# Optimization experiments

Measured on AMD Instinct MI355X. Metric: run time of the kernel, lower is better.

The kernel has to match this reference:

```python
import jax, jax.numpy as jnp
import numpy as np

N_NODES = 2000
GCN_OUT = 8
HID = 256
N_STEPS_OUT = 4


def setup_inputs() -> dict:
    key = jax.random.key(0)
    ks = jax.random.split(key, 16)
    B, S, N, E, F, H = 32, 24, N_NODES, 16000, GCN_OUT, HID
    I = F * N  # LSTM input size = gcn_out_features * num_nodes
    s = 0.05
    inp = {
        "x_sequences": jax.random.normal(ks[0], (B, S, N), jnp.float32),
        "edge_index": jax.random.randint(ks[1], (B, S, 2, E), 0, N, jnp.int32),
        "edge_distances": jax.random.uniform(ks[2], (B, S, E), jnp.float32),
        # CustomGCNLayer params (linear 1->F)
        "W_gcn": jax.random.normal(ks[3], (1, F), jnp.float32) * s,
        "b_gcn": jnp.zeros((F,), jnp.float32),
        # 2-layer LSTM (PyTorch layout: [4H, in], gate order i,f,g,o)
        "Wih0": jax.random.normal(ks[4], (4 * H, I), jnp.float32) * s,
        "Whh0": jax.random.normal(ks[5], (4 * H, H), jnp.float32) * s,
        "bih0": jnp.zeros((4 * H,), jnp.float32),
        "bhh0": jnp.zeros((4 * H,), jnp.float32),
        "Wih1": jax.random.normal(ks[6], (4 * H, H), jnp.float32) * s,
        "Whh1": jax.random.normal(ks[7], (4 * H, H), jnp.float32) * s,
        "bih1": jnp.zeros((4 * H,), jnp.float32),
        "bhh1": jnp.zeros((4 * H,), jnp.float32),
        # fc: hidden -> n_steps_out * num_nodes * num_node_features
        "fc_W": jax.random.normal(ks[8], (N_STEPS_OUT * N, H), jnp.float32) * s,
        "fc_b": jnp.zeros((N_STEPS_OUT * N,), jnp.float32),
    }
    return inp


def _lstm_layer(x, Wih, Whh, bih, bhh):
    # x: [B, S, in] -> hs: [B, S, H]
    B = x.shape[0]
    H = Whh.shape[1]
    b = bih + bhh

    def step(carry, xt):
        h, c = carry
        gates = xt @ Wih.T + h @ Whh.T + b  # [B, 4H]
        i, f, g, o = jnp.split(gates, 4, axis=-1)
        i = jax.nn.sigmoid(i)
        f = jax.nn.sigmoid(f)
        g = jnp.tanh(g)
        o = jax.nn.sigmoid(o)
        c = f * c + i * g
        h = o * jnp.tanh(c)
        return (h, c), h

    init = (jnp.zeros((B, H), x.dtype), jnp.zeros((B, H), x.dtype))
    _, hs = jax.lax.scan(step, init, x.transpose(1, 0, 2))  # time-major
    return hs.transpose(1, 0, 2)


def reference(x_sequences, edge_index, edge_distances, W_gcn, b_gcn,
              Wih0, Whh0, bih0, bhh0, Wih1, Whh1, bih1, bhh1, fc_W, fc_b):
    B, S, N = x_sequences.shape
    F = W_gcn.shape[1]
    # GCN layer (batched over all B*S graph snapshots):
    # h = x @ W + b ; out[i] = sum_{(j->i)} dist_e * h[j]
    h = x_sequences[..., None] * W_gcn[0] + b_gcn        # [B,S,N,F]
    src = edge_index[:, :, 0].reshape(B * S, -1)         # [BS,E]
    dst = edge_index[:, :, 1].reshape(B * S, -1)
    dist = edge_distances.reshape(B * S, -1)
    h2 = h.reshape(B * S, N, F)
    msgs = jnp.take_along_axis(h2, src[:, :, None], axis=1) * dist[..., None]  # [BS,E,F]
    agg = jax.vmap(lambda m, d: jax.ops.segment_sum(m, d, num_segments=N))(msgs, dst)
    gcn_seq = jnp.tanh(agg.reshape(B, S, N * F))         # [B,S,N*F]

    h1 = _lstm_layer(gcn_seq, Wih0, Whh0, bih0, bhh0)
    h2l = _lstm_layer(h1, Wih1, Whh1, bih1, bhh1)
    last = jnp.tanh(h2l)[:, -1, :]                       # [B,H]
    out = last @ fc_W.T + fc_b                           # [B, n_steps_out*N]
    n_steps_out = fc_b.shape[0] // N
    return out.reshape(B, n_steps_out, N)                # num_node_features=1 squeezed
```

## Files before the change

### kernel.cpp

```cpp
#include <hip/hip_runtime.h>

#define DEVINL __device__ __forceinline__

typedef __attribute__((ext_vector_type(8))) short bf16x8;
typedef __attribute__((ext_vector_type(4))) float f32x4;
typedef _Float16 half2_t __attribute__((ext_vector_type(2)));
typedef _Float16 f16x8 __attribute__((ext_vector_type(8)));

DEVINL unsigned short f2bf(float f) {
  unsigned int u = __float_as_uint(f);
  u += 0x7FFFu + ((u >> 16) & 1u);
  return (unsigned short)(u >> 16);
}
DEVINL float sigmf(float x) { return 1.f / (1.f + __expf(-x)); }
DEVINL float tanh_fast(float x) { float e = __expf(2.f * x); return 1.f - 2.f / (e + 1.f); }

DEVINL float fdot2u(unsigned int h, unsigned int w, float acc) {
  return __builtin_amdgcn_fdot2(__builtin_bit_cast(half2_t, h),
                                __builtin_bit_cast(half2_t, w), acc, false);
}


__global__ __launch_bounds__(256) void conv_bf16(const float* __restrict__ in,
                                                 unsigned short* __restrict__ out) {
  int id = blockIdx.x * 256 + threadIdx.x;
  float4 v = *(const float4*)&in[(size_t)id * 4];
  unsigned int a = (unsigned int)f2bf(v.x) | ((unsigned int)f2bf(v.y) << 16);
  unsigned int b = (unsigned int)f2bf(v.z) | ((unsigned int)f2bf(v.w) << 16);
  *(uint2*)&out[(size_t)id * 4] = make_uint2(a, b);
}

__global__ __launch_bounds__(256) void conv_f16(const float* __restrict__ in,
                                                unsigned short* __restrict__ out) {
  int id = blockIdx.x * 256 + threadIdx.x;
  out[id] = __builtin_bit_cast(unsigned short, (_Float16)in[id]);
}

__global__ __launch_bounds__(256) void pack_whh_f16(const float* __restrict__ in,
                                                    unsigned int* __restrict__ out) {
  int id = blockIdx.x * 256 + threadIdx.x;
  int t = id >> 8;
  int cs = (id >> 7) & 1;
  int u = id & 127;
  int col = t + cs * 512;
  float a = in[col * 256 + 2 * u];
  float b = in[col * 256 + 2 * u + 1];
  unsigned short ha = __builtin_bit_cast(unsigned short, (_Float16)a);
  unsigned short hb = __builtin_bit_cast(unsigned short, (_Float16)b);
  out[id] = (unsigned int)ha | ((unsigned int)hb << 16);
}

#define FXSCALE 1048576.f
#define FXINV   (1.f / 1048576.f)

__global__ __launch_bounds__(1024) void gcn_kernel(
    const float* __restrict__ x, const int* __restrict__ ei, const float* __restrict__ ed,
    const float* __restrict__ Wg, const float* __restrict__ bg,
    unsigned short* __restrict__ G) {
  __shared__ float xs[2000];
  __shared__ int Ai[2000];
  __shared__ int Di[2000];
  int bs = blockIdx.x;
  int tid = threadIdx.x;
  for (int i = tid; i < 2000; i += 1024) {
    xs[i] = x[(size_t)bs * 2000 + i];
    Ai[i] = 0; Di[i] = 0;
  }
  __syncthreads();
  const int* srcp = ei + (size_t)bs * 32000;
  const int* dstp = srcp + 16000;
  const float* dp = ed + (size_t)bs * 16000;
  for (int i = tid; i < 4000; i += 1024) {
    int4 s4 = ((const int4*)srcp)[i];
    int4 d4 = ((const int4*)dstp)[i];
    float4 w4 = ((const float4*)dp)[i];
    atomicAdd(&Ai[d4.x], __float2int_rn(w4.x * xs[s4.x] * FXSCALE));
    atomicAdd(&Di[d4.x], __float2int_rn(w4.x * FXSCALE));
    atomicAdd(&Ai[d4.y], __float2int_rn(w4.y * xs[s4.y] * FXSCALE));
    atomicAdd(&Di[d4.y], __float2int_rn(w4.y * FXSCALE));
    atomicAdd(&Ai[d4.z], __float2int_rn(w4.z * xs[s4.z] * FXSCALE));
    atomicAdd(&Di[d4.z], __float2int_rn(w4.z * FXSCALE));
    atomicAdd(&Ai[d4.w], __float2int_rn(w4.w * xs[s4.w] * FXSCALE));
    atomicAdd(&Di[d4.w], __float2int_rn(w4.w * FXSCALE));
  }
  __syncthreads();
  float wreg[8], breg[8];
#pragma unroll
  for (int f = 0; f < 8; ++f) { wreg[f] = Wg[f]; breg[f] = bg[f]; }
  for (int n = tid; n < 2000; n += 1024) {
    float a  = (float)Ai[n] * FXINV;
    float dd = (float)Di[n] * FXINV;
    unsigned int u[4];
#pragma unroll
    for (int p = 0; p < 4; ++p) {
      float v0 = tanh_fast(wreg[2 * p] * a + breg[2 * p] * dd);
      float v1 = tanh_fast(wreg[2 * p + 1] * a + breg[2 * p + 1] * dd);
      u[p] = (unsigned int)f2bf(v0) | ((unsigned int)f2bf(v1) << 16);
    }
    *(uint4*)&G[(size_t)bs * 16000 + n * 8] = make_uint4(u[0], u[1], u[2], u[3]);
  }
}

__global__ __launch_bounds__(256) void gemm_bt(
    const unsigned short* __restrict__ A, const unsigned short* __restrict__ B,
    float* __restrict__ Cp) {
  __shared__ __align__(16) unsigned short As[128 * 32];
  __shared__ __align__(16) unsigned short Bs[128 * 32];
  const int K = 16000;
  int nt = blockIdx.x;
  int mt = blockIdx.y;
  int ks = blockIdx.z;
  int m0 = mt * 128, n0 = nt * 128;
  int tid = threadIdx.x;
  int lane = tid & 63;
  int w = tid >> 6;
  int wm = (w >> 1) * 64, wn = (w & 1) * 64;
  int fr = lane & 15;
  int kg = lane >> 4;

  f32x4 acc[4][4] = {};
  const unsigned short* Ag = A + (size_t)m0 * K + ks * 1600;
  const unsigned short* Bg = B + (size_t)n0 * K + ks * 1600;

  for (int kk = 0; kk < 1600; kk += 32) {
#pragma unroll
    for (int q = 0; q < 2; ++q) {
      int c = q * 256 + tid;
      int row = c >> 2;
      int ko = (c & 3) * 8;
      *(uint4*)&As[c * 8] = *(const uint4*)&Ag[(size_t)row * K + kk + ko];
      *(uint4*)&Bs[c * 8] = *(const uint4*)&Bg[(size_t)row * K + kk + ko];
    }
    __syncthreads();
    bf16x8 aF[4], bF[4];
#pragma unroll
    for (int i = 0; i < 4; ++i)
      aF[i] = *(const bf16x8*)&As[(wm + i * 16 + fr) * 32 + kg * 8];
#pragma unroll
    for (int i = 0; i < 4; ++i)
      bF[i] = *(const bf16x8*)&Bs[(wn + i * 16 + fr) * 32 + kg * 8];
#pragma unroll
    for (int i = 0; i < 4; ++i)
#pragma unroll
      for (int j = 0; j < 4; ++j)
        acc[i][j] = __builtin_amdgcn_mfma_f32_16x16x32_bf16(aF[i], bF[j], acc[i][j], 0, 0, 0);
    __syncthreads();
  }
  float* Co = Cp + (size_t)ks * 768 * 1024;
  int mr = (lane >> 4) * 4;
#pragma unroll
  for (int i = 0; i < 4; ++i)
#pragma unroll
    for (int j = 0; j < 4; ++j) {
      int n = n0 + wn + j * 16 + fr;
#pragma unroll
      for (int r = 0; r < 4; ++r) {
        int m = m0 + wm + i * 16 + mr + r;
        Co[(size_t)m * 1024 + n] = acc[i][j][r];
      }
    }
}

__global__ __launch_bounds__(256) void reduce_z0(
    const float* __restrict__ Cp, const float* __restrict__ bih,
    const float* __restrict__ bhh, float* __restrict__ Z0) {
  int id = blockIdx.x * 256 + threadIdx.x;
  float s = bih[id & 1023] + bhh[id & 1023];
#pragma unroll
  for (int p = 0; p < 10; ++p) s += Cp[(size_t)p * 786432 + id];
  Z0[id] = s;
}

__global__ __launch_bounds__(512, 1) void lstm_fused(
    const float* __restrict__ Z, const unsigned int* __restrict__ WPK,
    unsigned short* __restrict__ Hout, float* __restrict__ lastOut) {
  __shared__ __align__(16) uint4 Wl4[18 * 512];
  __shared__ float g_lds[1024];
  __shared__ __align__(8) unsigned short h16[256];
  int b = blockIdx.x;
  int tid = threadIdx.x;
  int lane = tid & 63;

  unsigned int wr0[92], wr1[92];
  const uint4* wp = (const uint4*)(WPK + (size_t)tid * 256);
#pragma unroll
  for (int q = 0; q < 23; ++q) {
    uint4 v = wp[q];
    wr0[q * 4] = v.x; wr0[q * 4 + 1] = v.y; wr0[q * 4 + 2] = v.z; wr0[q * 4 + 3] = v.w;
  }
#pragma unroll
  for (int q = 0; q < 23; ++q) {
    uint4 v = wp[32 + q];
    wr1[q * 4] = v.x; wr1[q * 4 + 1] = v.y; wr1[q * 4 + 2] = v.z; wr1[q * 4 + 3] = v.w;
  }
#pragma unroll
  for (int g = 0; g < 9; ++g)
    Wl4[g * 512 + tid] = wp[23 + g];
#pragma unroll
  for (int g = 0; g < 9; ++g)
    Wl4[(9 + g) * 512 + tid] = wp[55 + g];
  if (tid < 128) ((unsigned int*)h16)[tid] = 0;
  __syncthreads();

  float cst = 0.f;
  const size_t b24 = (size_t)b * 24;
  const float* Zb = Z + b24 * 1024 + tid;

#pragma unroll 1
  for (int t = 0; t < 24; ++t) {
    uint2 hv = *(const uint2*)&((const unsigned int*)h16)[lane * 2];
    float z0 = Zb[t * 1024];
    float z1 = Zb[t * 1024 + 512];
    float a0a = 0.f, a0b = 0.f, a1a = 0.f, a1b = 0.f;
#pragma unroll
    for (int u = 0; u < 92; ++u) {
      unsigned int hu = (unsigned int)__builtin_amdgcn_readlane(
          (int)((u & 1) ? hv.y : hv.x), u >> 1);
      if (u & 1) { a0b = fdot2u(hu, wr0[u], a0b); a1b = fdot2u(hu, wr1[u], a1b); }
      else       { a0a = fdot2u(hu, wr0[u], a0a); a1a = fdot2u(hu, wr1[u], a1a); }
    }
#pragma unroll
    for (int g = 0; g < 9; ++g) {
      uint4 wa = Wl4[g * 512 + tid];
      uint4 wb = Wl4[(9 + g) * 512 + tid];
#pragma unroll
      for (int r = 0; r < 4; ++r) {
        const int u = 92 + g * 4 + r;
        unsigned int hu = (unsigned int)__builtin_amdgcn_readlane(
            (int)((u & 1) ? hv.y : hv.x), u >> 1);
        unsigned int w0r = (r == 0) ? wa.x : (r == 1) ? wa.y : (r == 2) ? wa.z : wa.w;
        unsigned int w1r = (r == 0) ? wb.x : (r == 1) ? wb.y : (r == 2) ? wb.z : wb.w;
        if (u & 1) { a0b = fdot2u(hu, w0r, a0b); a1b = fdot2u(hu, w1r, a1b); }
        else       { a0a = fdot2u(hu, w0r, a0a); a1a = fdot2u(hu, w1r, a1a); }
      }
    }
    g_lds[tid] = z0 + a0a + a0b;
    g_lds[tid + 512] = z1 + a1a + a1b;
    __syncthreads();
    if (tid < 256) {
      float ig = sigmf(g_lds[tid]);
      float fg = sigmf(g_lds[tid + 256]);
      float gg = tanh_fast(g_lds[tid + 512]);
      float og = sigmf(g_lds[tid + 768]);
      cst = fg * cst + ig * gg;
      float h = og * tanh_fast(cst);
      unsigned short hh = __builtin_bit_cast(unsigned short, (_Float16)h);
      h16[tid] = hh;
      if (Hout) Hout[(b24 + t) * 256 + tid] = hh;
      if (lastOut && t == 23) lastOut[b * 256 + tid] = tanh_fast(h);
    }
    __syncthreads();
  }
}

__global__ __launch_bounds__(256) void gemm_z1_mfma(
    const unsigned short* __restrict__ A, const unsigned short* __restrict__ B,
    const float* __restrict__ bih, const float* __restrict__ bhh,
    float* __restrict__ Z1) {
  __shared__ __align__(16) unsigned short As[128 * 32];
  __shared__ __align__(16) unsigned short Bs[128 * 32];
  const int K = 256;
  int nt = blockIdx.x;
  int mt = blockIdx.y;
  int m0 = mt * 128, n0 = nt * 128;
  int tid = threadIdx.x;
  int lane = tid & 63;
  int w = tid >> 6;
  int wm = (w >> 1) * 64, wn = (w & 1) * 64;
  int fr = lane & 15;
  int kg = lane >> 4;

  f32x4 acc[4][4] = {};
  const unsigned short* Ag = A + (size_t)m0 * K;
  const unsigned short* Bg = B + (size_t)n0 * K;

  for (int kk = 0; kk < 256; kk += 32) {
#pragma unroll
    for (int q = 0; q < 2; ++q) {
      int c = q * 256 + tid;
      int row = c >> 2;
      int ko = (c & 3) * 8;
      *(uint4*)&As[c * 8] = *(const uint4*)&Ag[(size_t)row * K + kk + ko];
      *(uint4*)&Bs[c * 8] = *(const uint4*)&Bg[(size_t)row * K + kk + ko];
    }
    __syncthreads();
    f16x8 aF[4], bF[4];
#pragma unroll
    for (int i = 0; i < 4; ++i)
      aF[i] = *(const f16x8*)&As[(wm + i * 16 + fr) * 32 + kg * 8];
#pragma unroll
    for (int i = 0; i < 4; ++i)
      bF[i] = *(const f16x8*)&Bs[(wn + i * 16 + fr) * 32 + kg * 8];
#pragma unroll
    for (int i = 0; i < 4; ++i)
#pragma unroll
      for (int j = 0; j < 4; ++j)
        acc[i][j] = __builtin_amdgcn_mfma_f32_16x16x32_f16(aF[i], bF[j], acc[i][j], 0, 0, 0);
    __syncthreads();
  }
  int mr = (lane >> 4) * 4;
#pragma unroll
  for (int j = 0; j < 4; ++j) {
    int n = n0 + wn + j * 16 + fr;
    float bias = bih[n] + bhh[n];
#pragma unroll
    for (int i = 0; i < 4; ++i) {
#pragma unroll
      for (int r = 0; r < 4; ++r) {
        int m = m0 + wm + i * 16 + mr + r;
        Z1[(size_t)m * 1024 + n] = acc[i][j][r] + bias;
      }
    }
  }
}

__global__ __launch_bounds__(256) void fc_kernel(
    const float* __restrict__ last, const float* __restrict__ fcW,
    const float* __restrict__ fcb, float* __restrict__ out) {
  __shared__ float ls[8][256];
  int tid = threadIdx.x;
  int o = blockIdx.x * 256 + tid;
  int b0 = blockIdx.y * 8;
  for (int i = tid; i < 2048; i += 256)
    ls[i >> 8][i & 255] = last[(b0 + (i >> 8)) * 256 + (i & 255)];
  __syncthreads();
  if (o < 8000) {
    float acc[8] = {};
    for (int k = 0; k < 256; k += 4) {
      float4 wv = *(const float4*)&fcW[(size_t)o * 256 + k];
#pragma unroll
      for (int b = 0; b < 8; ++b)
        acc[b] += wv.x * ls[b][k] + wv.y * ls[b][k + 1] + wv.z * ls[b][k + 2] + wv.w * ls[b][k + 3];
    }
    float bias = fcb[o];
#pragma unroll
    for (int b = 0; b < 8; ++b) out[(size_t)(b0 + b) * 8000 + o] = acc[b] + bias;
  }
}

extern "C" void kernel_launch(void* const* d_in, const int* in_sizes, int n_in,
                              void* d_out, int out_size, void* d_ws, size_t ws_size,
                              hipStream_t stream) {
  const float* x    = (const float*)d_in[0];
  const int*   ei   = (const int*)d_in[1];
  const float* ed   = (const float*)d_in[2];
  const float* Wg   = (const float*)d_in[3];
  const float* bg   = (const float*)d_in[4];
  const float* Wih0 = (const float*)d_in[5];
  const float* Whh0 = (const float*)d_in[6];
  const float* bih0 = (const float*)d_in[7];
  const float* bhh0 = (const float*)d_in[8];
  const float* Wih1 = (const float*)d_in[9];
  const float* Whh1 = (const float*)d_in[10];
  const float* bih1 = (const float*)d_in[11];
  const float* bhh1 = (const float*)d_in[12];
  const float* fcW  = (const float*)d_in[13];
  const float* fcb  = (const float*)d_in[14];
  float* out = (float*)d_out;

  char* ws = (char*)d_ws;
  unsigned short* Gbf  = (unsigned short*)(ws);
  unsigned short* W0bf = (unsigned short*)(ws + 24576000);
  float* Zpart = (float*)(ws + 57344000);
  float* Z0    = (float*)(ws + 88801280);
  unsigned int* WPK0 = (unsigned int*)(ws + 91947008);
  unsigned int* WPK1 = (unsigned int*)(ws + 92471296);
  unsigned short* W1h = (unsigned short*)(ws + 92995584);
  unsigned short* H1  = (unsigned short*)(ws + 94044160);
  float* Z1    = (float*)(ws + 94830592);
  float* lastb = (float*)(ws + 97976320);

  conv_bf16<<<16000, 256, 0, stream>>>(Wih0, W0bf);
  pack_whh_f16<<<512, 256, 0, stream>>>(Whh0, WPK0);
  pack_whh_f16<<<512, 256, 0, stream>>>(Whh1, WPK1);
  conv_f16<<<1024, 256, 0, stream>>>(Wih1, (unsigned short*)W1h);
  gcn_kernel<<<768, 1024, 0, stream>>>(x, ei, ed, Wg, bg, Gbf);
  gemm_bt<<<dim3(8, 6, 10), 256, 0, stream>>>(Gbf, W0bf, Zpart);
  reduce_z0<<<3072, 256, 0, stream>>>(Zpart, bih0, bhh0, Z0);
  lstm_fused<<<32, 512, 0, stream>>>(Z0, WPK0, H1, nullptr);
  gemm_z1_mfma<<<dim3(8, 6), 256, 0, stream>>>(H1, W1h, bih1, bhh1, Z1);
  lstm_fused<<<32, 512, 0, stream>>>(Z1, WPK1, nullptr, lastb);
  fc_kernel<<<dim3(32, 4), 256, 0, stream>>>(lastb, fcW, fcb, out);
}
```

Before: 284.2 us.

## Use one thread per gate column in LSTM recurrence with 1024-thread blocks

The recurrent LSTM kernel now runs 1024 threads per batch element, with each thread computing one gate column instead of two. Per-thread weight registers drop from 184 to 96, the LDS-resident portion shrinks to 8 uint4 per thread, and the packing kernel now stores rows in plain column order. The aim is to halve the serial dot-product chain per timestep, at the cost of 1024-thread blocks, tighter register limits and possibly more barrier overhead.

```diff
diff --git a/kernel.cpp b/kernel.cpp
--- a/kernel.cpp
+++ b/kernel.cpp
@@ -36,17 +36,14 @@
   out[id] = __builtin_bit_cast(unsigned short, (_Float16)in[id]);
 }
 
-__global__ __launch_bounds__(256) void pack_whh_f16(const float* __restrict__ in,
-                                                    unsigned int* __restrict__ out) {
+__global__ __launch_bounds__(256) void pack_whh_cols(const float* __restrict__ in,
+                                                     unsigned int* __restrict__ out) {
   int id = blockIdx.x * 256 + threadIdx.x;
-  int t = id >> 8;
-  int cs = (id >> 7) & 1;
+  int j = id >> 7;
   int u = id & 127;
-  int col = t + cs * 512;
-  float a = in[col * 256 + 2 * u];
-  float b = in[col * 256 + 2 * u + 1];
-  unsigned short ha = __builtin_bit_cast(unsigned short, (_Float16)a);
-  unsigned short hb = __builtin_bit_cast(unsigned short, (_Float16)b);
+  float2 v = *(const float2*)&in[j * 256 + 2 * u];
+  unsigned short ha = __builtin_bit_cast(unsigned short, (_Float16)v.x);
+  unsigned short hb = __builtin_bit_cast(unsigned short, (_Float16)v.y);
   out[id] = (unsigned int)ha | ((unsigned int)hb << 16);
 }
 
@@ -171,34 +168,26 @@
   Z0[id] = s;
 }
 
-__global__ __launch_bounds__(512, 1) void lstm_fused(
+__global__ __launch_bounds__(1024) void lstm_fused(
     const float* __restrict__ Z, const unsigned int* __restrict__ WPK,
     unsigned short* __restrict__ Hout, float* __restrict__ lastOut) {
-  __shared__ __align__(16) uint4 Wl4[18 * 512];
+  __shared__ __align__(16) uint4 Wl4[8 * 1024];
   __shared__ float g_lds[1024];
   __shared__ __align__(8) unsigned short h16[256];
   int b = blockIdx.x;
   int tid = threadIdx.x;
   int lane = tid & 63;
 
-  unsigned int wr0[92], wr1[92];
-  const uint4* wp = (const uint4*)(WPK + (size_t)tid * 256);
-#pragma unroll
-  for (int q = 0; q < 23; ++q) {
+  unsigned int wr[96];
+  const uint4* wp = (const uint4*)(WPK + (size_t)tid * 128);
+#pragma unroll
+  for (int q = 0; q < 24; ++q) {
     uint4 v = wp[q];
-    wr0[q * 4] = v.x; wr0[q * 4 + 1] = v.y; wr0[q * 4 + 2] = v.z; wr0[q * 4 + 3] = v.w;
-  }
-#pragma unroll
-  for (int q = 0; q < 23; ++q) {
-    uint4 v = wp[32 + q];
-    wr1[q * 4] = v.x; wr1[q * 4 + 1] = v.y; wr1[q * 4 + 2] = v.z; wr1[q * 4 + 3] = v.w;
-  }
-#pragma unroll
-  for (int g = 0; g < 9; ++g)
-    Wl4[g * 512 + tid] = wp[23 + g];
-#pragma unroll
-  for (int g = 0; g < 9; ++g)
-    Wl4[(9 + g) * 512 + tid] = wp[55 + g];
+    wr[q * 4] = v.x; wr[q * 4 + 1] = v.y; wr[q * 4 + 2] = v.z; wr[q * 4 + 3] = v.w;
+  }
+#pragma unroll
+  for (int g = 0; g < 8; ++g)
+    Wl4[g * 1024 + tid] = wp[24 + g];
   if (tid < 128) ((unsigned int*)h16)[tid] = 0;
   __syncthreads();
 
@@ -209,33 +198,29 @@
 #pragma unroll 1
   for (int t = 0; t < 24; ++t) {
     uint2 hv = *(const uint2*)&((const unsigned int*)h16)[lane * 2];
-    float z0 = Zb[t * 1024];
-    float z1 = Zb[t * 1024 + 512];
-    float a0a = 0.f, a0b = 0.f, a1a = 0.f, a1b = 0.f;
-#pragma unroll
-    for (int u = 0; u < 92; ++u) {
+    float z = Zb[t * 1024];
+    float ae = 0.f, ao = 0.f;
+#pragma unroll
+    for (int u = 0; u < 96; ++u) {
       unsigned int hu = (unsigned int)__builtin_amdgcn_readlane(
           (int)((u & 1) ? hv.y : hv.x), u >> 1);
-      if (u & 1) { a0b = fdot2u(hu, wr0[u], a0b); a1b = fdot2u(hu, wr1[u], a1b); }
-      else       { a0a = fdot2u(hu, wr0[u], a0a); a1a = fdot2u(hu, wr1[u], a1a); }
-    }
-#pragma unroll
-    for (int g = 0; g < 9; ++g) {
-      uint4 wa = Wl4[g * 512 + tid];
-      uint4 wb = Wl4[(9 + g) * 512 + tid];
+      if (u & 1) ao = fdot2u(hu, wr[u], ao);
+      else       ae = fdot2u(hu, wr[u], ae);
+    }
+#pragma unroll
+    for (int g = 0; g < 8; ++g) {
+      uint4 wa = Wl4[g * 1024 + tid];
 #pragma unroll
       for (int r = 0; r < 4; ++r) {
-        const int u = 92 + g * 4 + r;
+        const int u = 96 + g * 4 + r;
         unsigned int hu = (unsigned int)__builtin_amdgcn_readlane(
             (int)((u & 1) ? hv.y : hv.x), u >> 1);
-        unsigned int w0r = (r == 0) ? wa.x : (r == 1) ? wa.y : (r == 2) ? wa.z : wa.w;
-        unsigned int w1r = (r == 0) ? wb.x : (r == 1) ? wb.y : (r == 2) ? wb.z : wb.w;
-        if (u & 1) { a0b = fdot2u(hu, w0r, a0b); a1b = fdot2u(hu, w1r, a1b); }
-        else       { a0a = fdot2u(hu, w0r, a0a); a1a = fdot2u(hu, w1r, a1a); }
+        unsigned int wv = (r == 0) ? wa.x : (r == 1) ? wa.y : (r == 2) ? wa.z : wa.w;
+        if (u & 1) ao = fdot2u(hu, wv, ao);
+        else       ae = fdot2u(hu, wv, ae);
       }
     }
-    g_lds[tid] = z0 + a0a + a0b;
-    g_lds[tid + 512] = z1 + a1a + a1b;
+    g_lds[tid] = z + ae + ao;
     __syncthreads();
     if (tid < 256) {
       float ig = sigmf(g_lds[tid]);
@@ -371,14 +356,14 @@
   float* lastb = (float*)(ws + 97976320);
 
   conv_bf16<<<16000, 256, 0, stream>>>(Wih0, W0bf);
-  pack_whh_f16<<<512, 256, 0, stream>>>(Whh0, WPK0);
-  pack_whh_f16<<<512, 256, 0, stream>>>(Whh1, WPK1);
+  pack_whh_cols<<<512, 256, 0, stream>>>(Whh0, WPK0);
+  pack_whh_cols<<<512, 256, 0, stream>>>(Whh1, WPK1);
   conv_f16<<<1024, 256, 0, stream>>>(Wih1, (unsigned short*)W1h);
   gcn_kernel<<<768, 1024, 0, stream>>>(x, ei, ed, Wg, bg, Gbf);
   gemm_bt<<<dim3(8, 6, 10), 256, 0, stream>>>(Gbf, W0bf, Zpart);
   reduce_z0<<<3072, 256, 0, stream>>>(Zpart, bih0, bhh0, Z0);
-  lstm_fused<<<32, 512, 0, stream>>>(Z0, WPK0, H1, nullptr);
+  lstm_fused<<<32, 1024, 0, stream>>>(Z0, WPK0, H1, nullptr);
   gemm_z1_mfma<<<dim3(8, 6), 256, 0, stream>>>(H1, W1h, bih1, bhh1, Z1);
-  lstm_fused<<<32, 512, 0, stream>>>(Z1, WPK1, nullptr, lastb);
+  lstm_fused<<<32, 1024, 0, stream>>>(Z1, WPK1, nullptr, lastb);
   fc_kernel<<<dim3(32, 4), 256, 0, stream>>>(lastb, fcW, fcb, out);
 }
```

New measurement: 290.4 us. 1.02x slower.
